# Kernel tuning notes

Hardware: AMD Instinct MI355X
Metric: run time of the kernel (lower is better)

The kernel has to match this reference:

```python
import jax, jax.numpy as jnp
import numpy as np

DIM = 256
QK_DIM = 256
SCALE = QK_DIM ** (-0.5)


def depthwise_conv3x3(x_img, w, b):
    # x_img: [B, C, H, W], w: [C, 1, 3, 3] (OIHW, groups=C), b: [C]
    out = jax.lax.conv_general_dilated(
        x_img, w, window_strides=(1, 1), padding='SAME',
        feature_group_count=x_img.shape[1],
        dimension_numbers=('NCHW', 'OIHW', 'NCHW'))
    return out + b[None, :, None, None]


def setup_inputs() -> dict:
    key = jax.random.key(0)
    ks = jax.random.split(key, 7)
    B, N, C = 4, 4096, DIM
    s = 0.02
    return {
        'x': jax.random.normal(ks[0], (B, N, C), jnp.float32),
        'W_qkv': jax.random.normal(ks[1], (C, 3 * C), jnp.float32) * s,
        'W_gate': jax.random.normal(ks[2], (C, C), jnp.float32) * s,
        'b_gate': jax.random.normal(ks[3], (C,), jnp.float32) * s,
        'W_proj': jax.random.normal(ks[4], (C, C), jnp.float32) * s,
        'pe_w': jax.random.normal(ks[5], (C, 1, 3, 3), jnp.float32) * s,
        'pe_b': jax.random.normal(ks[6], (C,), jnp.float32) * s,
    }


def reference(x, W_qkv, W_gate, b_gate, W_proj, pe_w, pe_b):
    B, N, C = x.shape
    ws = int(N ** 0.5)
    qkv = x @ W_qkv                               # [B, N, 3C]
    q, k, v = jnp.split(qkv, [QK_DIM, 2 * QK_DIM], axis=-1)
    z = jax.nn.gelu(x @ W_gate + b_gate, approximate=False)  # [B, N, C]
    # depthwise-conv positional encoding on q viewed as an image
    q_img = jnp.transpose(q, (0, 2, 1)).reshape(B, C, ws, ws)
    pe = depthwise_conv3x3(q_img, pe_w, pe_b).reshape(B, C, N)
    pe = jnp.transpose(pe, (0, 2, 1))             # [B, N, C]
    # single-head attention (heads arg unused in the original forward)
    attn = jax.nn.softmax(jnp.einsum('bnc,bmc->bnm', q, k) * SCALE, axis=-1)
    out = jnp.einsum('bnm,bmc->bnc', attn, v) + pe
    out = out * z
    return out @ W_proj
```

## Files before the change

### kernel.cpp

```cpp
#include <hip/hip_runtime.h>
#include <hip/hip_bf16.h>
#include <math.h>
#include <stdint.h>

typedef unsigned short u16;
typedef __attribute__((ext_vector_type(8))) short bf8;
typedef __attribute__((ext_vector_type(4))) float f4;

#define SC_LOG2E 0.09016844f

__device__ __forceinline__ float b2f(u16 u) {
    union { uint32_t i; float f; } v; v.i = ((uint32_t)u) << 16; return v.f;
}
__device__ __forceinline__ u16 f2b(float f) {
    union { float f; uint32_t i; } v; v.f = f;
    uint32_t r = (v.i + 0x7FFFu + ((v.i >> 16) & 1u)) >> 16;
    return (u16)r;
}
__device__ __forceinline__ uint32_t pk_bf16(float lo, float hi) {
    uint32_t r;
    asm("v_cvt_pk_bf16_f32 %0, %1, %2" : "=v"(r) : "v"(lo), "v"(hi));
    return r;
}

__global__ __launch_bounds__(256) void prep_weights(
        const float* __restrict__ Wqkv, const float* __restrict__ Wgate,
        const float* __restrict__ Wproj,
        u16* __restrict__ WT_all, u16* __restrict__ WTp) {
    int e = blockIdx.x * 256 + threadIdx.x;
    if (e < 262144) {
        int n = e >> 8, k = e & 255;
        WT_all[e] = f2b((n < 768) ? Wqkv[k * 768 + n] : Wgate[k * 256 + (n - 768)]);
    } else {
        int e2 = e - 262144;
        int n = e2 >> 8, k = e2 & 255;
        WTp[e2] = f2b(Wproj[k * 256 + n]);
    }
}

__global__ __launch_bounds__(256) void xcast(
        const float* __restrict__ x, u16* __restrict__ xb) {
    int i = (blockIdx.x * 256 + threadIdx.x) * 4;
    float4 f = *(const float4*)&x[i];
    uint2 o;
    o.x = pk_bf16(f.x, f.y);
    o.y = pk_bf16(f.z, f.w);
    *(uint2*)&xb[i] = o;
}

__global__ __launch_bounds__(512) void gemm_qkvz(
        const u16* __restrict__ xb, const u16* __restrict__ WT,
        const float* __restrict__ b_gate,
        u16* __restrict__ qo, u16* __restrict__ ko,
        u16* __restrict__ vT, u16* __restrict__ zo) {
    __shared__ u16 As[128 * 64];
    __shared__ u16 Bs[256 * 64];
    const int t = threadIdx.x;
    const int w = t >> 6, lane = t & 63, l15 = lane & 15, q4 = lane >> 4;
    const int vrl = lane >> 3, vsl = lane & 7;
    const int m0 = blockIdx.x * 128;
    const int n0 = blockIdx.y * 256;

    f4 acc[16];
#pragma unroll
    for (int i = 0; i < 16; i++) acc[i] = (f4){0.f, 0.f, 0.f, 0.f};

    for (int kt = 0; kt < 4; ++kt) {
        __syncthreads();
#pragma unroll
        for (int j = 0; j < 2; j++) {
            int op = j * 8 + w;
            int r = op * 8 + vrl;
            int cn = (vsl - r) & 7;
            const u16* g = &xb[(size_t)(m0 + r) * 256 + kt * 64 + cn * 8];
            __builtin_amdgcn_global_load_lds(
                (const __attribute__((address_space(1))) unsigned int*)g,
                (__attribute__((address_space(3))) unsigned int*)&As[op * 512],
                16, 0, 0);
        }
#pragma unroll
        for (int j = 0; j < 4; j++) {
            int op = j * 8 + w;
            int r = op * 8 + vrl;
            int cn = (vsl - r) & 7;
            const u16* g = &WT[(size_t)(n0 + r) * 256 + kt * 64 + cn * 8];
            __builtin_amdgcn_global_load_lds(
                (const __attribute__((address_space(1))) unsigned int*)g,
                (__attribute__((address_space(3))) unsigned int*)&Bs[op * 512],
                16, 0, 0);
        }
        __syncthreads();
#pragma unroll
        for (int c = 0; c < 2; c++) {
            int Ra = w * 16 + l15;
            int slota = ((c * 4 + q4) + Ra) & 7;
            bf8 af = *(bf8*)&As[Ra * 64 + slota * 8];
#pragma unroll
            for (int nt = 0; nt < 16; nt++) {
                int R = nt * 16 + l15;
                int slot = ((c * 4 + q4) + R) & 7;
                bf8 bf = *(bf8*)&Bs[R * 64 + slot * 8];
                acc[nt] = __builtin_amdgcn_mfma_f32_16x16x32_bf16(af, bf, acc[nt], 0, 0, 0);
            }
        }
    }

    const int rb = m0 + w * 16 + q4 * 4;
    if (blockIdx.y == 0) {
#pragma unroll
        for (int nt = 0; nt < 16; nt++) {
            int col = nt * 16 + l15;
#pragma unroll
            for (int r = 0; r < 4; r++) qo[(rb + r) * 256 + col] = f2b(acc[nt][r]);
        }
    } else if (blockIdx.y == 1) {
#pragma unroll
        for (int nt = 0; nt < 16; nt++) {
            int col = nt * 16 + l15;
#pragma unroll
            for (int r = 0; r < 4; r++) ko[(rb + r) * 256 + col] = f2b(acc[nt][r]);
        }
    } else if (blockIdx.y == 2) {
        int bb = rb >> 12, nn = rb & 4095;
#pragma unroll
        for (int nt = 0; nt < 16; nt++) {
            int vc = nt * 16 + l15;
            ushort4 pk;
            pk.x = f2b(acc[nt][0]); pk.y = f2b(acc[nt][1]);
            pk.z = f2b(acc[nt][2]); pk.w = f2b(acc[nt][3]);
            *(ushort4*)&vT[(bb * 256 + vc) * 4096 + nn] = pk;
        }
    } else {
#pragma unroll
        for (int nt = 0; nt < 16; nt++) {
            int gc = nt * 16 + l15;
            float bg = b_gate[gc];
#pragma unroll
            for (int r = 0; r < 4; r++) {
                float v = acc[nt][r] + bg;
                float g = 0.5f * v * (1.0f + erff(v * 0.70710678118654752f));
                zo[(rb + r) * 256 + gc] = f2b(g);
            }
        }
    }
}

__global__ __launch_bounds__(256) void conv_pe(
        const u16* __restrict__ q, const float* __restrict__ pw,
        const float* __restrict__ pb, u16* __restrict__ pe) {
    const int bid = blockIdx.x;
    const int b = bid >> 8, h = (bid >> 2) & 63, wsg = bid & 3;
    const int c = threadIdx.x;
    float wgt[9];
#pragma unroll
    for (int i = 0; i < 9; i++) wgt[i] = pw[c * 9 + i];
    const float bias = pb[c];
    const u16* qb = q + b * (4096 * 256);
    u16* peb = pe + b * (4096 * 256);
    const bool vTop = h > 0, vBot = h < 63;
    const u16* rT = qb + (h - 1) * 64 * 256 + c;
    const u16* rM = qb + h * 64 * 256 + c;
    const u16* rB = qb + (h + 1) * 64 * 256 + c;
    const int w0 = wsg * 16;

    float t0, t1, t2, m0v, m1, m2, b0, b1, b2v;
    if (w0 > 0) {
        int o = (w0 - 1) * 256;
        t0 = vTop ? b2f(rT[o]) : 0.f;
        m0v = b2f(rM[o]);
        b0 = vBot ? b2f(rB[o]) : 0.f;
    } else { t0 = 0.f; m0v = 0.f; b0 = 0.f; }
    {
        int o = w0 * 256;
        t1 = vTop ? b2f(rT[o]) : 0.f;
        m1 = b2f(rM[o]);
        b1 = vBot ? b2f(rB[o]) : 0.f;
    }
#pragma unroll
    for (int w2 = 0; w2 < 16; ++w2) {
        int wn = w0 + w2 + 1;
        if (wn < 64) {
            int o = wn * 256;
            t2 = vTop ? b2f(rT[o]) : 0.f;
            m2 = b2f(rM[o]);
            b2v = vBot ? b2f(rB[o]) : 0.f;
        } else { t2 = 0.f; m2 = 0.f; b2v = 0.f; }
        float acc = bias
            + wgt[0] * t0 + wgt[1] * t1 + wgt[2] * t2
            + wgt[3] * m0v + wgt[4] * m1 + wgt[5] * m2
            + wgt[6] * b0 + wgt[7] * b1 + wgt[8] * b2v;
        peb[(h * 64 + w0 + w2) * 256 + c] = f2b(acc);
        t0 = t1; t1 = t2; m0v = m1; m1 = m2; b0 = b1; b1 = b2v;
    }
}

__global__ __launch_bounds__(512) void attn(
        const u16* __restrict__ q, const u16* __restrict__ k,
        const u16* __restrict__ vT, const u16* __restrict__ pe,
        const u16* __restrict__ z, u16* __restrict__ u) {
    __shared__ u16 Kst[32 * 520];
    __shared__ u16 Vs2[2][256 * 64];
    __shared__ u16 Ps[64 * 72];
    __shared__ float l_part[8][64];

    const int t = threadIdx.x;
    const int w = t >> 6, lane = t & 63, l15 = lane & 15, q4 = lane >> 4;
    const int kg = w >> 1, qh = w & 1;
    const int xcd = blockIdx.x & 7;
    const int b = xcd >> 1;
    const int qt = (blockIdx.x >> 3) * 2 + (xcd & 1);
    const int m0 = b * 4096 + qt * 64;

    const u16* kb = k + (size_t)b * 4096 * 256;
    const u16* vbase = vT + (size_t)b * 256 * 4096;

    const int lo = lane >> 5;
    const int lcn = ((lane & 31) - 4 * lo) & 31;

    auto stage64 = [&](const u16* src) {
#pragma unroll
        for (int rr = 0; rr < 4; rr++) {
            int pp = rr * 8 + w;
            const u16* g = src + (size_t)(pp * 2 + lo) * 256 + lcn * 8;
            u16* l = &Kst[pp * 520];
            __builtin_amdgcn_global_load_lds(
                (const __attribute__((address_space(1))) unsigned int*)g,
                (__attribute__((address_space(3))) unsigned int*)l, 16, 0, 0);
        }
    };
    const int vrl = lane >> 3, vsl = lane & 7;
    auto stageV = [&](const u16* src, u16* dst) {
#pragma unroll
        for (int j = 0; j < 4; j++) {
            int op = j * 8 + w;
            int r = op * 8 + vrl;
            int cn = (vsl - r) & 7;
            const u16* g = src + (size_t)r * 4096 + cn * 8;
            u16* l = dst + op * 512;
            __builtin_amdgcn_global_load_lds(
                (const __attribute__((address_space(1))) unsigned int*)g,
                (__attribute__((address_space(3))) unsigned int*)l, 16, 0, 0);
        }
    };
    auto kaddr = [&](int row, int cn) -> const u16* {
        int o = row & 1;
        return &Kst[(row >> 1) * 520 + o * 256 + (((cn + 4 * o) & 31) << 3)];
    };

    stage64(q + (size_t)m0 * 256);
    __syncthreads();
    bf8 qf[2][8];
#pragma unroll
    for (int qtt = 0; qtt < 2; qtt++)
#pragma unroll
        for (int c = 0; c < 8; c++)
            qf[qtt][c] = *(const bf8*)kaddr(qh * 32 + qtt * 16 + l15, c * 4 + q4);
    __syncthreads();

    stage64(kb);
    stageV(vbase, Vs2[0]);

    f4 O[2][4];
#pragma unroll
    for (int vg = 0; vg < 2; vg++)
#pragma unroll
        for (int qg = 0; qg < 4; qg++) O[vg][qg] = (f4){0.f, 0.f, 0.f, 0.f};
    float lrow[2] = {0.f, 0.f};

    auto body = [&](int kt, const u16* Vcur, u16* Vnxt) {
        __syncthreads();

        f4 St[2];
        St[0] = (f4){0.f, 0.f, 0.f, 0.f};
        St[1] = (f4){0.f, 0.f, 0.f, 0.f};
        __builtin_amdgcn_s_setprio(1);
#pragma unroll
        for (int c = 0; c < 8; c++) {
            bf8 kf = *(const bf8*)kaddr(kg * 16 + l15, c * 4 + q4);
            St[0] = __builtin_amdgcn_mfma_f32_16x16x32_bf16(kf, qf[0][c], St[0], 0, 0, 0);
            St[1] = __builtin_amdgcn_mfma_f32_16x16x32_bf16(kf, qf[1][c], St[1], 0, 0, 0);
        }
        __builtin_amdgcn_s_setprio(0);

#pragma unroll
        for (int qtt = 0; qtt < 2; qtt++) {
            float e0 = exp2f(fminf(fmaxf(St[qtt][0] * SC_LOG2E, -30.f), 30.f));
            float e1 = exp2f(fminf(fmaxf(St[qtt][1] * SC_LOG2E, -30.f), 30.f));
            float e2 = exp2f(fminf(fmaxf(St[qtt][2] * SC_LOG2E, -30.f), 30.f));
            float e3 = exp2f(fminf(fmaxf(St[qtt][3] * SC_LOG2E, -30.f), 30.f));
            uint2 pk;
            pk.x = pk_bf16(e0, e1);
            pk.y = pk_bf16(e2, e3);
            int qrow = qh * 32 + qtt * 16 + l15;
            *(uint2*)&Ps[qrow * 72 + kg * 16 + q4 * 4] = pk;
            float s = (e0 + e1) + (e2 + e3);
            s += __shfl_xor(s, 16);
            s += __shfl_xor(s, 32);
            lrow[qtt] += s;
        }
        __syncthreads();

        if (kt < 63) {
            stage64(kb + (size_t)(kt + 1) * 16384);
            stageV(vbase + (size_t)(kt + 1) * 64, Vnxt);
        }

        bf8 pf[4][2], vfr[2][2];
#pragma unroll
        for (int qg = 0; qg < 4; qg++)
#pragma unroll
            for (int kh = 0; kh < 2; kh++)
                pf[qg][kh] = *(bf8*)&Ps[(qg * 16 + l15) * 72 + kh * 32 + q4 * 8];
#pragma unroll
        for (int vg = 0; vg < 2; vg++)
#pragma unroll
            for (int kh = 0; kh < 2; kh++) {
                int R = w * 32 + vg * 16 + l15;
                int slot = ((kh * 4 + q4) + R) & 7;
                vfr[vg][kh] = *(const bf8*)&Vcur[R * 64 + slot * 8];
            }
        __builtin_amdgcn_s_setprio(1);
#pragma unroll
        for (int vg = 0; vg < 2; vg++)
#pragma unroll
            for (int qg = 0; qg < 4; qg++) {
                O[vg][qg] = __builtin_amdgcn_mfma_f32_16x16x32_bf16(
                    vfr[vg][0], pf[qg][0], O[vg][qg], 0, 0, 0);
                O[vg][qg] = __builtin_amdgcn_mfma_f32_16x16x32_bf16(
                    vfr[vg][1], pf[qg][1], O[vg][qg], 0, 0, 0);
            }
        __builtin_amdgcn_s_setprio(0);
    };

    for (int kt2 = 0; kt2 < 64; kt2 += 2) {
        body(kt2,     Vs2[0], Vs2[1]);
        body(kt2 + 1, Vs2[1], Vs2[0]);
    }

    if (q4 == 0) {
        l_part[w][qh * 32 + l15] = lrow[0];
        l_part[w][qh * 32 + 16 + l15] = lrow[1];
    }
    __syncthreads();

#pragma unroll
    for (int qg = 0; qg < 4; qg++) {
        int qrow = qg * 16 + l15;
        int qhq = qg >> 1;
        float lt = l_part[qhq][qrow] + l_part[2 + qhq][qrow]
                 + l_part[4 + qhq][qrow] + l_part[6 + qhq][qrow];
        float linv = 1.0f / lt;
        size_t mrow = (size_t)(m0 + qrow) * 256;
#pragma unroll
        for (int vg = 0; vg < 2; vg++) {
            int vcb = w * 32 + vg * 16 + q4 * 4;
            ushort4 pe4 = *(const ushort4*)&pe[mrow + vcb];
            ushort4 z4  = *(const ushort4*)&z[mrow + vcb];
            float r0 = (O[vg][qg][0] * linv + b2f(pe4.x)) * b2f(z4.x);
            float r1 = (O[vg][qg][1] * linv + b2f(pe4.y)) * b2f(z4.y);
            float r2 = (O[vg][qg][2] * linv + b2f(pe4.z)) * b2f(z4.z);
            float r3 = (O[vg][qg][3] * linv + b2f(pe4.w)) * b2f(z4.w);
            uint2 o4;
            o4.x = pk_bf16(r0, r1);
            o4.y = pk_bf16(r2, r3);
            *(uint2*)&u[mrow + vcb] = o4;
        }
    }
}

__global__ __launch_bounds__(256) void gemm_proj(
        const u16* __restrict__ u, const u16* __restrict__ WTp,
        float* __restrict__ out) {
    __shared__ u16 As[64 * 64];
    __shared__ u16 Bs[256 * 64];
    const int t = threadIdx.x;
    const int w = t >> 6, lane = t & 63, l15 = lane & 15, q4 = lane >> 4;
    const int vrl = lane >> 3, vsl = lane & 7;
    const int m0 = blockIdx.x * 64;

    f4 acc[16];
#pragma unroll
    for (int i = 0; i < 16; i++) acc[i] = (f4){0.f, 0.f, 0.f, 0.f};

    for (int kt = 0; kt < 4; ++kt) {
        __syncthreads();
#pragma unroll
        for (int j = 0; j < 2; j++) {
            int op = j * 4 + w;
            int r = op * 8 + vrl;
            int cn = (vsl - r) & 7;
            const u16* g = &u[(size_t)(m0 + r) * 256 + kt * 64 + cn * 8];
            __builtin_amdgcn_global_load_lds(
                (const __attribute__((address_space(1))) unsigned int*)g,
                (__attribute__((address_space(3))) unsigned int*)&As[op * 512],
                16, 0, 0);
        }
#pragma unroll
        for (int j = 0; j < 8; j++) {
            int op = j * 4 + w;
            int r = op * 8 + vrl;
            int cn = (vsl - r) & 7;
            const u16* g = &WTp[(size_t)r * 256 + kt * 64 + cn * 8];
            __builtin_amdgcn_global_load_lds(
                (const __attribute__((address_space(1))) unsigned int*)g,
                (__attribute__((address_space(3))) unsigned int*)&Bs[op * 512],
                16, 0, 0);
        }
        __syncthreads();
#pragma unroll
        for (int c = 0; c < 2; c++) {
            int Ra = w * 16 + l15;
            int slota = ((c * 4 + q4) + Ra) & 7;
            bf8 af = *(bf8*)&As[Ra * 64 + slota * 8];
#pragma unroll
            for (int nt = 0; nt < 16; nt++) {
                int R = nt * 16 + l15;
                int slot = ((c * 4 + q4) + R) & 7;
                bf8 bf = *(bf8*)&Bs[R * 64 + slot * 8];
                acc[nt] = __builtin_amdgcn_mfma_f32_16x16x32_bf16(af, bf, acc[nt], 0, 0, 0);
            }
        }
    }
    const int rb = m0 + w * 16 + q4 * 4;
#pragma unroll
    for (int nt = 0; nt < 16; nt++) {
        int col = nt * 16 + l15;
#pragma unroll
        for (int r = 0; r < 4; r++) out[(rb + r) * 256 + col] = acc[nt][r];
    }
}

extern "C" void kernel_launch(void* const* d_in, const int* in_sizes, int n_in,
                              void* d_out, int out_size, void* d_ws, size_t ws_size,
                              hipStream_t stream) {
    (void)in_sizes; (void)n_in; (void)out_size; (void)ws_size;
    const float* x      = (const float*)d_in[0];
    const float* Wqkv   = (const float*)d_in[1];
    const float* Wgate  = (const float*)d_in[2];
    const float* bgate  = (const float*)d_in[3];
    const float* Wproj  = (const float*)d_in[4];
    const float* pw     = (const float*)d_in[5];
    const float* pb     = (const float*)d_in[6];
    float* out = (float*)d_out;

    char* ws = (char*)d_ws;
    u16* WT_all = (u16*)(ws);
    u16* WTp    = (u16*)(ws + 524288);
    u16* q      = (u16*)(ws + 655360);
    u16* k      = (u16*)(ws + 9043968);
    u16* vT     = (u16*)(ws + 17432576);
    u16* z      = (u16*)(ws + 25821184);
    u16* pe     = (u16*)(ws + 34209792);
    u16* u      = (u16*)(ws + 42598400);

    u16* xb = u;

    prep_weights<<<1280, 256, 0, stream>>>(Wqkv, Wgate, Wproj, WT_all, WTp);
    xcast<<<4096, 256, 0, stream>>>(x, xb);
    gemm_qkvz<<<dim3(128, 4), 512, 0, stream>>>(xb, WT_all, bgate, q, k, vT, z);
    conv_pe<<<1024, 256, 0, stream>>>(q, pw, pb, pe);
    attn<<<256, 512, 0, stream>>>(q, k, vT, pe, z, u);
    gemm_proj<<<256, 256, 0, stream>>>(u, WTp, out);
}
```

Measured before the change: 229.3 us.

## Retile QKVZ and projection GEMMs to 128x128 tiles with full-K LDS staging

Both GEMMs now use 128x128 output tiles: the whole K=256 slab of each operand is loaded into padded LDS in one pass, replacing the 4-step K loop and its barriers. Each wave computes a 32x64 sub-tile, and MFMA operand order is swapped for the row-major outputs so stores become vectorized 8-byte (bf16) or 16-byte (float) writes. The grid doubles to 128x8 for QKVZ, and the projection becomes 128x2 with 512 threads. This cuts per-thread accumulator registers and adds parallelism, at the cost of about 130KB of LDS per block, which limits occupancy.

```diff
diff --git a/kernel.cpp b/kernel.cpp
--- a/kernel.cpp
+++ b/kernel.cpp
@@ -53,93 +53,120 @@
         const float* __restrict__ b_gate,
         u16* __restrict__ qo, u16* __restrict__ ko,
         u16* __restrict__ vT, u16* __restrict__ zo) {
-    __shared__ u16 As[128 * 64];
-    __shared__ u16 Bs[256 * 64];
+    __shared__ u16 As[64 * 520];
+    __shared__ u16 Bs[64 * 520];
     const int t = threadIdx.x;
     const int w = t >> 6, lane = t & 63, l15 = lane & 15, q4 = lane >> 4;
-    const int vrl = lane >> 3, vsl = lane & 7;
     const int m0 = blockIdx.x * 128;
-    const int n0 = blockIdx.y * 256;
-
-    f4 acc[16];
-#pragma unroll
-    for (int i = 0; i < 16; i++) acc[i] = (f4){0.f, 0.f, 0.f, 0.f};
-
-    for (int kt = 0; kt < 4; ++kt) {
-        __syncthreads();
-#pragma unroll
-        for (int j = 0; j < 2; j++) {
-            int op = j * 8 + w;
-            int r = op * 8 + vrl;
-            int cn = (vsl - r) & 7;
-            const u16* g = &xb[(size_t)(m0 + r) * 256 + kt * 64 + cn * 8];
+    const int by = blockIdx.y;
+    const int n0 = by * 128;
+
+    const int lo = lane >> 5;
+    const int lcn = ((lane & 31) - 4 * lo) & 31;
+
+    auto stage128 = [&](const u16* src, u16* dst) {
+#pragma unroll
+        for (int rr = 0; rr < 8; rr++) {
+            int pp = rr * 8 + w;
+            const u16* g = src + (size_t)(pp * 2 + lo) * 256 + lcn * 8;
             __builtin_amdgcn_global_load_lds(
                 (const __attribute__((address_space(1))) unsigned int*)g,
-                (__attribute__((address_space(3))) unsigned int*)&As[op * 512],
+                (__attribute__((address_space(3))) unsigned int*)&dst[pp * 520],
                 16, 0, 0);
         }
-#pragma unroll
-        for (int j = 0; j < 4; j++) {
-            int op = j * 8 + w;
-            int r = op * 8 + vrl;
-            int cn = (vsl - r) & 7;
-            const u16* g = &WT[(size_t)(n0 + r) * 256 + kt * 64 + cn * 8];
-            __builtin_amdgcn_global_load_lds(
-                (const __attribute__((address_space(1))) unsigned int*)g,
-                (__attribute__((address_space(3))) unsigned int*)&Bs[op * 512],
-                16, 0, 0);
-        }
-        __syncthreads();
-#pragma unroll
-        for (int c = 0; c < 2; c++) {
-            int Ra = w * 16 + l15;
-            int slota = ((c * 4 + q4) + Ra) & 7;
-            bf8 af = *(bf8*)&As[Ra * 64 + slota * 8];
-#pragma unroll
-            for (int nt = 0; nt < 16; nt++) {
-                int R = nt * 16 + l15;
-                int slot = ((c * 4 + q4) + R) & 7;
-                bf8 bf = *(bf8*)&Bs[R * 64 + slot * 8];
-                acc[nt] = __builtin_amdgcn_mfma_f32_16x16x32_bf16(af, bf, acc[nt], 0, 0, 0);
-            }
-        }
-    }
-
-    const int rb = m0 + w * 16 + q4 * 4;
-    if (blockIdx.y == 0) {
-#pragma unroll
-        for (int nt = 0; nt < 16; nt++) {
-            int col = nt * 16 + l15;
-#pragma unroll
-            for (int r = 0; r < 4; r++) qo[(rb + r) * 256 + col] = f2b(acc[nt][r]);
-        }
-    } else if (blockIdx.y == 1) {
-#pragma unroll
-        for (int nt = 0; nt < 16; nt++) {
-            int col = nt * 16 + l15;
-#pragma unroll
-            for (int r = 0; r < 4; r++) ko[(rb + r) * 256 + col] = f2b(acc[nt][r]);
-        }
-    } else if (blockIdx.y == 2) {
-        int bb = rb >> 12, nn = rb & 4095;
-#pragma unroll
-        for (int nt = 0; nt < 16; nt++) {
-            int vc = nt * 16 + l15;
-            ushort4 pk;
-            pk.x = f2b(acc[nt][0]); pk.y = f2b(acc[nt][1]);
-            pk.z = f2b(acc[nt][2]); pk.w = f2b(acc[nt][3]);
-            *(ushort4*)&vT[(bb * 256 + vc) * 4096 + nn] = pk;
+    };
+    auto kaddr = [&](const u16* base, int row, int cn) -> const u16* {
+        int o = row & 1;
+        return base + (row >> 1) * 520 + o * 256 + (((cn + 4 * o) & 31) << 3);
+    };
+
+    stage128(&xb[(size_t)m0 * 256], As);
+    stage128(&WT[(size_t)n0 * 256], Bs);
+    __syncthreads();
+
+    const int mtb = (w & 3) * 32;
+    const int ntb = (w >> 2) * 64;
+    const bool vTout = (by >> 1) == 2;
+
+    f4 acc[2][4];
+#pragma unroll
+    for (int i = 0; i < 2; i++)
+#pragma unroll
+        for (int j = 0; j < 4; j++) acc[i][j] = (f4){0.f, 0.f, 0.f, 0.f};
+
+#pragma unroll
+    for (int c = 0; c < 8; c++) {
+        bf8 af0 = *(const bf8*)kaddr(As, mtb + l15, c * 4 + q4);
+        bf8 af1 = *(const bf8*)kaddr(As, mtb + 16 + l15, c * 4 + q4);
+        if (vTout) {
+#pragma unroll
+            for (int j = 0; j < 4; j++) {
+                bf8 bfj = *(const bf8*)kaddr(Bs, ntb + j * 16 + l15, c * 4 + q4);
+                acc[0][j] = __builtin_amdgcn_mfma_f32_16x16x32_bf16(af0, bfj, acc[0][j], 0, 0, 0);
+                acc[1][j] = __builtin_amdgcn_mfma_f32_16x16x32_bf16(af1, bfj, acc[1][j], 0, 0, 0);
+            }
+        } else {
+#pragma unroll
+            for (int j = 0; j < 4; j++) {
+                bf8 bfj = *(const bf8*)kaddr(Bs, ntb + j * 16 + l15, c * 4 + q4);
+                acc[0][j] = __builtin_amdgcn_mfma_f32_16x16x32_bf16(bfj, af0, acc[0][j], 0, 0, 0);
+                acc[1][j] = __builtin_amdgcn_mfma_f32_16x16x32_bf16(bfj, af1, acc[1][j], 0, 0, 0);
+            }
+        }
+    }
+
+    const int kind = by >> 1;
+    const int colbase = (by & 1) * 128;
+
+    if (kind == 2) {
+        int bb = m0 >> 12;
+        int nnb = (m0 & 4095) + mtb + q4 * 4;
+#pragma unroll
+        for (int i = 0; i < 2; i++) {
+            int nn = nnb + i * 16;
+#pragma unroll
+            for (int j = 0; j < 4; j++) {
+                int vc = colbase + ntb + j * 16 + l15;
+                uint2 pk;
+                pk.x = pk_bf16(acc[i][j][0], acc[i][j][1]);
+                pk.y = pk_bf16(acc[i][j][2], acc[i][j][3]);
+                *(uint2*)&vT[(size_t)(bb * 256 + vc) * 4096 + nn] = pk;
+            }
+        }
+    } else if (kind == 3) {
+#pragma unroll
+        for (int i = 0; i < 2; i++) {
+            size_t mrow = (size_t)(m0 + mtb + i * 16 + l15) * 256 + colbase;
+#pragma unroll
+            for (int j = 0; j < 4; j++) {
+                int col = ntb + j * 16 + q4 * 4;
+                float4 bg4 = *(const float4*)&b_gate[colbase + col];
+                float v0 = acc[i][j][0] + bg4.x;
+                float v1 = acc[i][j][1] + bg4.y;
+                float v2 = acc[i][j][2] + bg4.z;
+                float v3 = acc[i][j][3] + bg4.w;
+                v0 = 0.5f * v0 * (1.0f + erff(v0 * 0.70710678118654752f));
+                v1 = 0.5f * v1 * (1.0f + erff(v1 * 0.70710678118654752f));
+                v2 = 0.5f * v2 * (1.0f + erff(v2 * 0.70710678118654752f));
+                v3 = 0.5f * v3 * (1.0f + erff(v3 * 0.70710678118654752f));
+                uint2 o;
+                o.x = pk_bf16(v0, v1);
+                o.y = pk_bf16(v2, v3);
+                *(uint2*)&zo[mrow + col] = o;
+            }
         }
     } else {
-#pragma unroll
-        for (int nt = 0; nt < 16; nt++) {
-            int gc = nt * 16 + l15;
-            float bg = b_gate[gc];
-#pragma unroll
-            for (int r = 0; r < 4; r++) {
-                float v = acc[nt][r] + bg;
-                float g = 0.5f * v * (1.0f + erff(v * 0.70710678118654752f));
-                zo[(rb + r) * 256 + gc] = f2b(g);
+        u16* dst = (kind == 0) ? qo : ko;
+#pragma unroll
+        for (int i = 0; i < 2; i++) {
+            size_t mrow = (size_t)(m0 + mtb + i * 16 + l15) * 256 + colbase;
+#pragma unroll
+            for (int j = 0; j < 4; j++) {
+                int col = ntb + j * 16 + q4 * 4;
+                uint2 o;
+                o.x = pk_bf16(acc[i][j][0], acc[i][j][1]);
+                o.y = pk_bf16(acc[i][j][2], acc[i][j][3]);
+                *(uint2*)&dst[mrow + col] = o;
             }
         }
     }
@@ -368,65 +395,67 @@
     }
 }
 
-__global__ __launch_bounds__(256) void gemm_proj(
+__global__ __launch_bounds__(512) void gemm_proj(
         const u16* __restrict__ u, const u16* __restrict__ WTp,
         float* __restrict__ out) {
-    __shared__ u16 As[64 * 64];
-    __shared__ u16 Bs[256 * 64];
+    __shared__ u16 As[64 * 520];
+    __shared__ u16 Bs[64 * 520];
     const int t = threadIdx.x;
     const int w = t >> 6, lane = t & 63, l15 = lane & 15, q4 = lane >> 4;
-    const int vrl = lane >> 3, vsl = lane & 7;
-    const int m0 = blockIdx.x * 64;
-
-    f4 acc[16];
-#pragma unroll
-    for (int i = 0; i < 16; i++) acc[i] = (f4){0.f, 0.f, 0.f, 0.f};
-
-    for (int kt = 0; kt < 4; ++kt) {
-        __syncthreads();
-#pragma unroll
-        for (int j = 0; j < 2; j++) {
-            int op = j * 4 + w;
-            int r = op * 8 + vrl;
-            int cn = (vsl - r) & 7;
-            const u16* g = &u[(size_t)(m0 + r) * 256 + kt * 64 + cn * 8];
+    const int m0 = blockIdx.x * 128;
+    const int n0 = blockIdx.y * 128;
+
+    const int lo = lane >> 5;
+    const int lcn = ((lane & 31) - 4 * lo) & 31;
+
+    auto stage128 = [&](const u16* src, u16* dst) {
+#pragma unroll
+        for (int rr = 0; rr < 8; rr++) {
+            int pp = rr * 8 + w;
+            const u16* g = src + (size_t)(pp * 2 + lo) * 256 + lcn * 8;
             __builtin_amdgcn_global_load_lds(
                 (const __attribute__((address_space(1))) unsigned int*)g,
-                (__attribute__((address_space(3))) unsigned int*)&As[op * 512],
+                (__attribute__((address_space(3))) unsigned int*)&dst[pp * 520],
                 16, 0, 0);
         }
-#pragma unroll
-        for (int j = 0; j < 8; j++) {
-            int op = j * 4 + w;
-            int r = op * 8 + vrl;
-            int cn = (vsl - r) & 7;
-            const u16* g = &WTp[(size_t)r * 256 + kt * 64 + cn * 8];
-            __builtin_amdgcn_global_load_lds(
-                (const __attribute__((address_space(1))) unsigned int*)g,
-                (__attribute__((address_space(3))) unsigned int*)&Bs[op * 512],
-                16, 0, 0);
-        }
-        __syncthreads();
-#pragma unroll
-        for (int c = 0; c < 2; c++) {
-            int Ra = w * 16 + l15;
-            int slota = ((c * 4 + q4) + Ra) & 7;
-            bf8 af = *(bf8*)&As[Ra * 64 + slota * 8];
-#pragma unroll
-            for (int nt = 0; nt < 16; nt++) {
-                int R = nt * 16 + l15;
-                int slot = ((c * 4 + q4) + R) & 7;
-                bf8 bf = *(bf8*)&Bs[R * 64 + slot * 8];
-                acc[nt] = __builtin_amdgcn_mfma_f32_16x16x32_bf16(af, bf, acc[nt], 0, 0, 0);
-            }
-        }
-    }
-    const int rb = m0 + w * 16 + q4 * 4;
-#pragma unroll
-    for (int nt = 0; nt < 16; nt++) {
-        int col = nt * 16 + l15;
-#pragma unroll
-        for (int r = 0; r < 4; r++) out[(rb + r) * 256 + col] = acc[nt][r];
+    };
+    auto kaddr = [&](const u16* base, int row, int cn) -> const u16* {
+        int o = row & 1;
+        return base + (row >> 1) * 520 + o * 256 + (((cn + 4 * o) & 31) << 3);
+    };
+
+    stage128(&u[(size_t)m0 * 256], As);
+    stage128(&WTp[(size_t)n0 * 256], Bs);
+    __syncthreads();
+
+    const int mtb = (w & 3) * 32;
+    const int ntb = (w >> 2) * 64;
+
+    f4 acc[2][4];
+#pragma unroll
+    for (int i = 0; i < 2; i++)
+#pragma unroll
+        for (int j = 0; j < 4; j++) acc[i][j] = (f4){0.f, 0.f, 0.f, 0.f};
+
+#pragma unroll
+    for (int c = 0; c < 8; c++) {
+        bf8 af0 = *(const bf8*)kaddr(As, mtb + l15, c * 4 + q4);
+        bf8 af1 = *(const bf8*)kaddr(As, mtb + 16 + l15, c * 4 + q4);
+#pragma unroll
+        for (int j = 0; j < 4; j++) {
+            bf8 bfj = *(const bf8*)kaddr(Bs, ntb + j * 16 + l15, c * 4 + q4);
+            acc[0][j] = __builtin_amdgcn_mfma_f32_16x16x32_bf16(bfj, af0, acc[0][j], 0, 0, 0);
+            acc[1][j] = __builtin_amdgcn_mfma_f32_16x16x32_bf16(bfj, af1, acc[1][j], 0, 0, 0);
+        }
+    }
+
+#pragma unroll
+    for (int i = 0; i < 2; i++) {
+        float* orow = &out[(size_t)(m0 + mtb + i * 16 + l15) * 256 + n0];
+#pragma unroll
+        for (int j = 0; j < 4; j++) {
+            *(f4*)&orow[ntb + j * 16 + q4 * 4] = acc[i][j];
+        }
     }
 }
 
@@ -457,8 +486,8 @@
 
     prep_weights<<<1280, 256, 0, stream>>>(Wqkv, Wgate, Wproj, WT_all, WTp);
     xcast<<<4096, 256, 0, stream>>>(x, xb);
-    gemm_qkvz<<<dim3(128, 4), 512, 0, stream>>>(xb, WT_all, bgate, q, k, vT, z);
+    gemm_qkvz<<<dim3(128, 8), 512, 0, stream>>>(xb, WT_all, bgate, q, k, vT, z);
     conv_pe<<<1024, 256, 0, stream>>>(q, pw, pb, pe);
     attn<<<256, 512, 0, stream>>>(q, k, vT, pe, z, u);
-    gemm_proj<<<256, 256, 0, stream>>>(u, WTp, out);
-}
+    gemm_proj<<<dim3(128, 2), 512, 0, stream>>>(u, WTp, out);
+}
```

After: 232.2 us. About the same (+1.3%).
